# Kernel tuning notes

Measured on AMD Instinct MI355X. Metric: run time of the kernel, lower is better.

## Reference

```python
import jax, jax.numpy as jnp
import numpy as np

N_NODES = 40000
N_EDGES = 100000
N_GRAPHS = 1024
C = 32          # output_channels
F_ATOM = 30     # NUMBER_ATOMIC_GRAPH_FEATURES
F_BOND = 11     # NUMBER_BOND_GRAPH_FEATURES
H_EDGE = 128    # hidden width of edge MLP (== batch_size arg)
T = 3           # num_iterations (message passing steps and set2set steps)


def setup_inputs() -> dict:
    key = jax.random.key(0)
    ks = jax.random.split(key, 16)
    s = lambda i, shape, sc=0.1: jax.random.normal(ks[i], shape, jnp.float32) * sc
    return {
        "x": jax.random.normal(ks[0], (N_NODES, F_ATOM), jnp.float32),
        "edge_attr": jax.random.normal(ks[1], (N_EDGES, F_BOND), jnp.float32),
        "edge_index": jax.random.randint(ks[2], (2, N_EDGES), 0, N_NODES),
        "batch": jnp.sort(jax.random.randint(ks[3], (N_NODES,), 0, N_GRAPHS)),
        "lin0_W": s(4, (C, F_ATOM)), "lin0_b": jnp.zeros((C,), jnp.float32),
        "mlp_W1": s(5, (H_EDGE, F_BOND)), "mlp_b1": jnp.zeros((H_EDGE,), jnp.float32),
        "mlp_W2": s(6, (C * C, H_EDGE), 0.02), "mlp_b2": jnp.zeros((C * C,), jnp.float32),
        "root_W": s(7, (C, C)), "conv_b": jnp.zeros((C,), jnp.float32),
        "gru_Wih": s(8, (3 * C, C)), "gru_Whh": s(9, (3 * C, C)),
        "gru_bih": jnp.zeros((3 * C,), jnp.float32), "gru_bhh": jnp.zeros((3 * C,), jnp.float32),
        "lstm_Wih": s(10, (4 * C, 2 * C)), "lstm_Whh": s(11, (4 * C, C)),
        "lstm_bih": jnp.zeros((4 * C,), jnp.float32), "lstm_bhh": jnp.zeros((4 * C,), jnp.float32),
        "lin1_W": s(12, (C, 2 * C)), "lin1_b": jnp.zeros((C,), jnp.float32),
        "lin2_W": s(13, (1, C)), "lin2_b": jnp.zeros((1,), jnp.float32),
    }


def _mpnn(x, edge_attr, lin0_W, lin0_b, mlp_W1, mlp_b1, mlp_W2, mlp_b2,
          root_W, conv_b, gru_Wih, gru_Whh, gru_bih, gru_bhh,
          lstm_Wih, lstm_Whh, lstm_bih, lstm_bhh, lin1_W, lin1_b, lin2_W, lin2_b,
          edge_index, batch):
    src, dst = edge_index[0], edge_index[1]
    out = jax.nn.relu(x @ lin0_W.T + lin0_b)          # [N, C]
    h = out                                           # GRU hidden state
    # edge-conditioned weights (edge_attr is constant across iterations)
    eh = jax.nn.relu(edge_attr @ mlp_W1.T + mlp_b1)
    W_e = (eh @ mlp_W2.T + mlp_b2).reshape(-1, C, C)  # [E, C, C]
    deg = jax.ops.segment_sum(jnp.ones((src.shape[0],), out.dtype), dst, N_NODES)
    denom = jnp.maximum(deg, 1.0)[:, None]
    for _ in range(T):
        # NNConv: gather + per-edge matmul + scatter-mean, plus root weight & bias
        msg = jnp.einsum('ec,eco->eo', out[src], W_e)               # [E, C]
        aggr = jax.ops.segment_sum(msg, dst, N_NODES) / denom       # mean aggr
        m = jax.nn.relu(aggr + out @ root_W + conv_b)
        # single GRU step (torch gate order r, z, n)
        gx = m @ gru_Wih.T + gru_bih
        gh = h @ gru_Whh.T + gru_bhh
        r = jax.nn.sigmoid(gx[:, :C] + gh[:, :C])
        z = jax.nn.sigmoid(gx[:, C:2 * C] + gh[:, C:2 * C])
        n = jnp.tanh(gx[:, 2 * C:] + r * gh[:, 2 * C:])
        h = (1.0 - z) * n + z * h
        out = h
    # Set2Set pooling (torch LSTM gate order i, f, g, o)
    q_star = jnp.zeros((N_GRAPHS, 2 * C), out.dtype)
    hs = jnp.zeros((N_GRAPHS, C), out.dtype)
    cs = jnp.zeros((N_GRAPHS, C), out.dtype)
    for _ in range(T):
        g = q_star @ lstm_Wih.T + lstm_bih + hs @ lstm_Whh.T + lstm_bhh
        i = jax.nn.sigmoid(g[:, :C])
        f = jax.nn.sigmoid(g[:, C:2 * C])
        gg = jnp.tanh(g[:, 2 * C:3 * C])
        o = jax.nn.sigmoid(g[:, 3 * C:])
        cs = f * cs + i * gg
        hs = o * jnp.tanh(cs)                                       # q, [B, C]
        e = jnp.sum(out * hs[batch], axis=-1)                       # [N]
        emax = jax.ops.segment_max(e, batch, N_GRAPHS)
        ee = jnp.exp(e - emax[batch])
        a = ee / jax.ops.segment_sum(ee, batch, N_GRAPHS)[batch]    # segment softmax
        rr = jax.ops.segment_sum(a[:, None] * out, batch, N_GRAPHS)
        q_star = jnp.concatenate([hs, rr], axis=-1)
    y = jax.nn.relu(q_star @ lin1_W.T + lin1_b)
    return y @ lin2_W.T + lin2_b                                    # [B, num_labels]


def reference(x, edge_index, edge_attr, batch, lin0_W, lin0_b, mlp_W1, mlp_b1,
              mlp_W2, mlp_b2, root_W, conv_b, gru_Wih, gru_Whh, gru_bih, gru_bhh,
              lstm_Wih, lstm_Whh, lstm_bih, lstm_bhh, lin1_W, lin1_b, lin2_W, lin2_b):
    return _mpnn(x, edge_attr, lin0_W, lin0_b, mlp_W1, mlp_b1, mlp_W2, mlp_b2,
                 root_W, conv_b, gru_Wih, gru_Whh, gru_bih, gru_bhh,
                 lstm_Wih, lstm_Whh, lstm_bih, lstm_bhh, lin1_W, lin1_b,
                 lin2_W, lin2_b, edge_index, batch)
```

## Files before the change

### kernel.cpp

```cpp
#include <hip/hip_runtime.h>
#include <hip/hip_bf16.h>
#include <cstdint>

#define NN 40000
#define NE 100000
#define NEP 100096
#define NB 1024
#define MAXN 192

typedef _Float16 halfT;
typedef _Float16 half8 __attribute__((ext_vector_type(8)));
typedef float f32x4 __attribute__((ext_vector_type(4)));

static __device__ __forceinline__ float sigf(float x){ return 1.f/(1.f + __expf(-x)); }
static __device__ __forceinline__ float tanh_f(float x){ float e = __expf(2.f * x); return 1.f - 2.f/(e + 1.f); }

__global__ __launch_bounds__(256) void k_zero(float4* __restrict__ p, int n4){
    int i = blockIdx.x * 256 + threadIdx.x;
    if (i < n4) p[i] = make_float4(0.f, 0.f, 0.f, 0.f);
}

__global__ __launch_bounds__(256) void k_setup(
    const float* __restrict__ x, const float* __restrict__ lin0_W, const float* __restrict__ lin0_b,
    const float* __restrict__ ea, const float* __restrict__ W1, const float* __restrict__ b1,
    const float* __restrict__ W2, const float* __restrict__ b2,
    const int* __restrict__ dstA, const int* __restrict__ batch,
    const float* __restrict__ rootW,
    const float* __restrict__ gWih, const float* __restrict__ gWhh,
    const float* __restrict__ lWih, const float* __restrict__ lWhh, const float* __restrict__ lin1_W,
    float* __restrict__ h, halfT* __restrict__ hH, halfT* __restrict__ ehF, halfT* __restrict__ BfF,
    float* __restrict__ deg, halfT* __restrict__ gateB,
    float* __restrict__ lWihT, float* __restrict__ lWhhT, float* __restrict__ lin1T,
    int* __restrict__ starts)
{
    int b = blockIdx.x, tid = threadIdx.x;
    if (b < 1250){
        __shared__ float sW[32 * 30];
        __shared__ float sB[32];
        for (int idx = tid; idx < 960; idx += 256) sW[idx] = lin0_W[idx];
        if (tid < 32) sB[tid] = lin0_b[tid];
        __syncthreads();
        int t8 = b * 256 + tid;
        int i = t8 >> 3, q4 = t8 & 7;
        const float* xr = x + (size_t)i * 30;
        float xv[30];
        #pragma unroll
        for (int f = 0; f < 30; f++) xv[f] = xr[f];
        float r[4];
        #pragma unroll
        for (int cc = 0; cc < 4; cc++){
            int c = q4 * 4 + cc;
            const float* wr = &sW[c * 30];
            float s = sB[c];
            #pragma unroll
            for (int f = 0; f < 30; f++) s += xv[f] * wr[f];
            r[cc] = fmaxf(s, 0.f);
        }
        *(float4*)(h + (size_t)i * 32 + q4 * 4) = *(float4*)r;
        halfT rh[4];
        #pragma unroll
        for (int cc = 0; cc < 4; cc++) rh[cc] = (halfT)r[cc];
        *(uint2*)(hH + (size_t)i * 32 + q4 * 4) = *(uint2*)rh;
    } else if (b < 7506){
        __shared__ float sW1[128 * 11];
        __shared__ float sb1[128];
        for (int idx = tid; idx < 1408; idx += 256) sW1[idx] = W1[idx];
        if (tid < 128) sb1[tid] = b1[tid];
        __syncthreads();
        int t8 = (b - 1250) * 256 + tid;
        int ch = t8 & 63;
        int s4 = (t8 >> 6) & 3;
        int g16 = t8 >> 8;
        int m = ch & 15, q = ch >> 4;
        int e = g16 * 16 + m;
        int kb = 32 * s4 + q * 8;
        halfT v[8];
        if (e < NE){
            const float* xr = ea + (size_t)e * 11;
            float xv[11];
            #pragma unroll
            for (int f = 0; f < 11; f++) xv[f] = xr[f];
            #pragma unroll
            for (int i8 = 0; i8 < 8; i8++){
                int k = kb + i8;
                const float* wr = &sW1[k * 11];
                float s = sb1[k];
                #pragma unroll
                for (int f = 0; f < 11; f++) s += xv[f] * wr[f];
                v[i8] = (halfT)fmaxf(s, 0.f);
            }
        } else {
            #pragma unroll
            for (int i8 = 0; i8 < 8; i8++) v[i8] = (halfT)0.f;
        }
        *(half8*)(ehF + (size_t)t8 * 8) = *(half8*)v;
    } else if (b < 8022){
        int gid = (b - 7506) * 256 + tid;
        int i8 = gid & 7;
        int ch = (gid >> 3) & 63;
        int nt = (gid >> 9) & 1;
        int ks = gid >> 10;
        int m = ch & 15, q = ch >> 4;
        int o = nt * 16 + m;
        float v;
        if (ks < 128){
            int c = ks >> 2;
            int k = 32 * (ks & 3) + q * 8 + i8;
            v = W2[(size_t)(c * 32 + o) * 128 + k];
        } else {
            int c = q * 8 + i8;
            v = b2[c * 32 + o];
        }
        BfF[gid] = (halfT)v;
    } else if (b < 8413){
        int e = (b - 8022) * 256 + tid;
        if (e < NE) atomicAdd(&deg[dstA[e]], 1.f);
    } else if (b < 8493){
        int t = (b - 8413) * 256 + tid;
        if (t < 8192){ int k = t >> 7, j = t & 127; lWihT[t] = lWih[(size_t)j * 64 + k]; }
        else if (t < 12288){ int t2 = t - 8192; int k = t2 >> 7, j = t2 & 127; lWhhT[t2] = lWhh[(size_t)j * 32 + k]; }
        else if (t < 14336){ int t2 = t - 12288; int k = t2 >> 5, c = t2 & 31; lin1T[t2] = lin1_W[(size_t)c * 64 + k]; }
    } else if (b < 8498){
        int g = (b - 8493) * 256 + tid;
        if (g > NB) return;
        int lo = 0, hi = NN;
        while (lo < hi){
            int mid = (lo + hi) >> 1;
            if (batch[mid] < g) lo = mid + 1; else hi = mid;
        }
        starts[g] = lo;
    } else {
        int t = (b - 8498) * 256 + tid;
        if (t >= 7168) return;
        int tile = t >> 9;
        int l = (t >> 3) & 63;
        int i = t & 7;
        int m = l & 15, q = l >> 4;
        int k = q * 8 + i;
        float v;
        if (tile < 2){
            int c = tile * 16 + m;
            v = rootW[(size_t)k * 32 + c];
        } else if (tile < 8){
            int j = (tile - 2) * 16 + m;
            v = gWih[(size_t)j * 32 + k];
        } else {
            int j = (tile - 8) * 16 + m;
            v = gWhh[(size_t)j * 32 + k];
        }
        gateB[t] = (halfT)v;
    }
}

__global__ __launch_bounds__(512, 4) void k_msg4(
    const halfT* __restrict__ ehF, const halfT* __restrict__ BfF,
    const halfT* __restrict__ hH,
    const int* __restrict__ src, const int* __restrict__ dst,
    float* __restrict__ aggr)
{
    __shared__ halfT sB[2][16384];
    int tid = threadIdx.x;
    int l = tid & 63;
    int wid = blockIdx.x * 8 + (tid >> 6);
    int m = l & 15, q = l >> 4;
    int eb = wid * 32;
    half8 pre[4];
    #pragma unroll
    for (int p = 0; p < 4; p++)
        pre[p] = *(const half8*)(BfF + (size_t)(p * 512 + tid) * 8);
    #pragma unroll
    for (int p = 0; p < 4; p++)
        *(half8*)(&sB[0][(p * 512 + tid) * 8]) = pre[p];
    half8 u0[4], u1[4], ub0, ub1;
    {
        int e0 = eb + m;      int se0 = (e0 < NE) ? src[e0] : 0;
        int e1 = eb + 16 + m; int se1 = (e1 < NE) ? src[e1] : 0;
        const halfT* p0 = hH + (size_t)se0 * 32;
        const halfT* p1 = hH + (size_t)se1 * 32;
        #pragma unroll
        for (int j = 0; j < 4; j++){
            u0[j] = *(const half8*)(p0 + j * 8);
            u1[j] = *(const half8*)(p1 + j * 8);
        }
        ub0 = *(const half8*)(p0 + q * 8);
        ub1 = *(const half8*)(p1 + q * 8);
    }
    half8 eh0[4], eh1[4];
    {
        int g0 = eb >> 4;
        #pragma unroll
        for (int s = 0; s < 4; s++){
            eh0[s] = *(const half8*)(ehF + ((size_t)(g0 * 4 + s) * 64 + l) * 8);
            eh1[s] = *(const half8*)(ehF + ((size_t)((g0 + 1) * 4 + s) * 64 + l) * 8);
        }
    }
    __syncthreads();
    #pragma unroll
    for (int p = 0; p < 4; p++)
        pre[p] = *(const half8*)(BfF + (size_t)16384 + (size_t)(p * 512 + tid) * 8);
    f32x4 acc00 = {0,0,0,0}, acc01 = {0,0,0,0}, acc10 = {0,0,0,0}, acc11 = {0,0,0,0};
    #pragma unroll
    for (int g = 0; g < 8; g++){
        const int cur = g & 1;
        #pragma unroll
        for (int j = 0; j < 16; j++){
            const int ks = g * 16 + j;
            half8 b0 = *(const half8*)(&sB[cur][(j * 2 + 0) * 512 + l * 8]);
            half8 b1 = *(const half8*)(&sB[cur][(j * 2 + 1) * 512 + l * 8]);
            const int c = ks >> 2, s = ks & 3;
            halfT uc0 = u0[c >> 3][c & 7];
            halfT uc1 = u1[c >> 3][c & 7];
            half8 a0 = eh0[s] * uc0;
            half8 a1 = eh1[s] * uc1;
            acc00 = __builtin_amdgcn_mfma_f32_16x16x32_f16(a0, b0, acc00, 0, 0, 0);
            acc01 = __builtin_amdgcn_mfma_f32_16x16x32_f16(a0, b1, acc01, 0, 0, 0);
            acc10 = __builtin_amdgcn_mfma_f32_16x16x32_f16(a1, b0, acc10, 0, 0, 0);
            acc11 = __builtin_amdgcn_mfma_f32_16x16x32_f16(a1, b1, acc11, 0, 0, 0);
        }
        if (g + 1 < 8){
            #pragma unroll
            for (int p = 0; p < 4; p++)
                *(half8*)(&sB[cur ^ 1][(p * 512 + tid) * 8]) = pre[p];
            if (g + 2 < 8){
                #pragma unroll
                for (int p = 0; p < 4; p++)
                    pre[p] = *(const half8*)(BfF + (size_t)(g + 2) * 16384 + (size_t)(p * 512 + tid) * 8);
            }
        }
        __syncthreads();
    }
    {
        half8 b0 = *(const half8*)(BfF + (size_t)256 * 512 + l * 8);
        half8 b1 = *(const half8*)(BfF + (size_t)257 * 512 + l * 8);
        acc00 = __builtin_amdgcn_mfma_f32_16x16x32_f16(ub0, b0, acc00, 0, 0, 0);
        acc01 = __builtin_amdgcn_mfma_f32_16x16x32_f16(ub0, b1, acc01, 0, 0, 0);
        acc10 = __builtin_amdgcn_mfma_f32_16x16x32_f16(ub1, b0, acc10, 0, 0, 0);
        acc11 = __builtin_amdgcn_mfma_f32_16x16x32_f16(ub1, b1, acc11, 0, 0, 0);
    }
    #pragma unroll
    for (int r = 0; r < 4; r++){
        int ea0 = eb + q * 4 + r;
        if (ea0 < NE){
            int d = dst[ea0];
            atomicAdd(&aggr[(size_t)d * 32 + m],      acc00[r]);
            atomicAdd(&aggr[(size_t)d * 32 + 16 + m], acc01[r]);
        }
        int ea1 = eb + 16 + q * 4 + r;
        if (ea1 < NE){
            int d = dst[ea1];
            atomicAdd(&aggr[(size_t)d * 32 + m],      acc10[r]);
            atomicAdd(&aggr[(size_t)d * 32 + 16 + m], acc11[r]);
        }
    }
}

__global__ __launch_bounds__(256) void k_gru(
    float* __restrict__ aggr, const float* __restrict__ deg,
    float* __restrict__ h, halfT* __restrict__ hH,
    const halfT* __restrict__ gateB,
    const float* __restrict__ gbih, const float* __restrict__ gbhh,
    const float* __restrict__ cb)
{
    __shared__ float hbuf[4][16][33];
    __shared__ float mbuf[4][16][33];
    int tid = threadIdx.x;
    int w = tid >> 6, l = tid & 63;
    int m16 = l & 15, q = l >> 4;
    int nb = blockIdx.x * 64 + w * 16;
    float hv[8];
    const float* hp = h + (size_t)(nb + m16) * 32 + q * 8;
    *(float4*)&hv[0] = *(const float4*)(hp);
    *(float4*)&hv[4] = *(const float4*)(hp + 4);
    half8 h_hi, h_lo;
    #pragma unroll
    for (int i = 0; i < 8; i++){
        halfT hi = (halfT)hv[i];
        h_hi[i] = hi;
        h_lo[i] = (halfT)(hv[i] - (float)hi);
        hbuf[w][m16][q * 8 + i] = hv[i];
    }
    f32x4 macc0 = {0,0,0,0}, macc1 = {0,0,0,0};
    {
        half8 B0 = *(const half8*)(gateB + ((size_t)0 * 64 + l) * 8);
        half8 B1 = *(const half8*)(gateB + ((size_t)1 * 64 + l) * 8);
        macc0 = __builtin_amdgcn_mfma_f32_16x16x32_f16(h_hi, B0, macc0, 0, 0, 0);
        macc0 = __builtin_amdgcn_mfma_f32_16x16x32_f16(h_lo, B0, macc0, 0, 0, 0);
        macc1 = __builtin_amdgcn_mfma_f32_16x16x32_f16(h_hi, B1, macc1, 0, 0, 0);
        macc1 = __builtin_amdgcn_mfma_f32_16x16x32_f16(h_lo, B1, macc1, 0, 0, 0);
    }
    {
        float cb0 = cb[m16], cb1 = cb[16 + m16];
        #pragma unroll
        for (int r = 0; r < 4; r++){
            int nr = q * 4 + r;
            int node = nb + nr;
            float invd = 1.f / fmaxf(deg[node], 1.f);
            size_t a0 = (size_t)node * 32 + m16;
            size_t a1 = a0 + 16;
            float av0 = aggr[a0]; aggr[a0] = 0.f;
            float av1 = aggr[a1]; aggr[a1] = 0.f;
            float mv0 = fmaxf(macc0[r] + av0 * invd + cb0, 0.f);
            float mv1 = fmaxf(macc1[r] + av1 * invd + cb1, 0.f);
            mbuf[w][nr][m16]      = mv0;
            mbuf[w][nr][16 + m16] = mv1;
        }
    }
    __syncthreads();
    half8 m_hi, m_lo;
    #pragma unroll
    for (int i = 0; i < 8; i++){
        float mval = mbuf[w][m16][q * 8 + i];
        halfT hi = (halfT)mval;
        m_hi[i] = hi;
        m_lo[i] = (halfT)(mval - (float)hi);
    }
    f32x4 gx[6], gh[6];
    #pragma unroll
    for (int t = 0; t < 6; t++){ gx[t] = (f32x4){0,0,0,0}; gh[t] = (f32x4){0,0,0,0}; }
    #pragma unroll
    for (int t = 0; t < 6; t++){
        half8 Bx = *(const half8*)(gateB + ((size_t)(2 + t) * 64 + l) * 8);
        half8 Bh = *(const half8*)(gateB + ((size_t)(8 + t) * 64 + l) * 8);
        gx[t] = __builtin_amdgcn_mfma_f32_16x16x32_f16(m_hi, Bx, gx[t], 0, 0, 0);
        gx[t] = __builtin_amdgcn_mfma_f32_16x16x32_f16(m_lo, Bx, gx[t], 0, 0, 0);
        gh[t] = __builtin_amdgcn_mfma_f32_16x16x32_f16(h_hi, Bh, gh[t], 0, 0, 0);
        gh[t] = __builtin_amdgcn_mfma_f32_16x16x32_f16(h_lo, Bh, gh[t], 0, 0, 0);
    }
    #pragma unroll
    for (int t = 0; t < 2; t++){
        int c = t * 16 + m16;
        float bxr = gbih[c],      bhr = gbhh[c];
        float bxz = gbih[32 + c], bhz = gbhh[32 + c];
        float bxn = gbih[64 + c], bhn = gbhh[64 + c];
        #pragma unroll
        for (int r = 0; r < 4; r++){
            int nr = q * 4 + r;
            int node = nb + nr;
            float rr = sigf(gx[t][r] + bxr + gh[t][r] + bhr);
            float zz = sigf(gx[2 + t][r] + bxz + gh[2 + t][r] + bhz);
            float nn = tanh_f(gx[4 + t][r] + bxn + rr * (gh[4 + t][r] + bhn));
            float hq = hbuf[w][nr][c];
            float hnew = (1.f - zz) * nn + zz * hq;
            h[(size_t)node * 32 + c]  = hnew;
            hH[(size_t)node * 32 + c] = (halfT)hnew;
        }
    }
}

__global__ __launch_bounds__(64) void k_s2s(
    const float* __restrict__ h, const int* __restrict__ starts,
    const float* __restrict__ lWihT, const float* __restrict__ lWhhT,
    const float* __restrict__ lbih, const float* __restrict__ lbhh,
    const float* __restrict__ lin1T, const float* __restrict__ lin1_b,
    const float* __restrict__ lin2W, const float* __restrict__ lin2b,
    float* __restrict__ e_buf, float* __restrict__ out)
{
    __shared__ float hl[MAXN * 33];
    __shared__ float al[MAXN];
    __shared__ float hsl[32];
    int g = blockIdx.x, l = threadIdx.x;
    int s0 = starts[g], s1 = starts[g + 1];
    int n = s1 - s0;
    int c = l & 31, grp = l >> 5;
    int nl = (n < MAXN) ? n : MAXN;
    for (int idx = l; idx < nl * 32; idx += 64)
        hl[(idx >> 5) * 33 + (idx & 31)] = h[(size_t)s0 * 32 + idx];
    __syncthreads();
    float qs = 0.f, hsv = 0.f, csv = 0.f;
    for (int t = 0; t < 3; t++){
        float a1 = lbih[l] + lbhh[l];
        float a2 = lbih[l + 64] + lbhh[l + 64];
        #pragma unroll 8
        for (int k = 0; k < 64; k++){
            float qk = __shfl(qs, k);
            a1 += qk * lWihT[k * 128 + l];
            a2 += qk * lWihT[k * 128 + 64 + l];
        }
        #pragma unroll 8
        for (int k = 0; k < 32; k++){
            float hk = __shfl(qs, k);
            a1 += hk * lWhhT[k * 128 + l];
            a2 += hk * lWhhT[k * 128 + 64 + l];
        }
        float gate1 = sigf(a1);
        float gate2 = (l < 32) ? tanhf(a2) : sigf(a2);
        float fv = __shfl(gate1, c + 32);
        float ov = __shfl(gate2, c + 32);
        if (l < 32){
            csv = fv * csv + gate1 * gate2;
            hsv = ov * tanhf(csv);
            hsl[l] = hsv;
        }
        __syncthreads();
        float lmax = -3.4e38f;
        for (int i = l; i < n; i += 64){
            const float* hr = (i < MAXN) ? &hl[i * 33] : &h[(size_t)(s0 + i) * 32];
            float p = 0.f;
            #pragma unroll
            for (int c2 = 0; c2 < 32; c2++) p += hr[c2] * hsl[c2];
            if (i < MAXN) al[i] = p; else e_buf[s0 + i] = p;
            lmax = fmaxf(lmax, p);
        }
        #pragma unroll
        for (int o = 1; o < 64; o <<= 1) lmax = fmaxf(lmax, __shfl_xor(lmax, o));
        float lsum = 0.f;
        for (int i = l; i < n; i += 64){
            float e = (i < MAXN) ? al[i] : e_buf[s0 + i];
            float a = expf(e - lmax);
            if (i < MAXN) al[i] = a; else e_buf[s0 + i] = a;
            lsum += a;
        }
        #pragma unroll
        for (int o = 1; o < 64; o <<= 1) lsum += __shfl_xor(lsum, o);
        float inv = (lsum > 0.f) ? 1.f / lsum : 0.f;
        __syncthreads();
        float acc = 0.f;
        for (int i = grp; i < n; i += 2){
            float a = (i < MAXN) ? al[i] : e_buf[s0 + i];
            const float* hr = (i < MAXN) ? &hl[i * 33] : &h[(size_t)(s0 + i) * 32];
            acc += a * hr[c];
        }
        acc *= inv;
        acc += __shfl_xor(acc, 32);
        qs = (l < 32) ? hsv : acc;
        __syncthreads();
    }
    float s = lin1_b[c];
    #pragma unroll 8
    for (int k = 0; k < 64; k++){
        float qk = __shfl(qs, k);
        s += qk * lin1T[k * 32 + c];
    }
    float pp = (l < 32) ? fmaxf(s, 0.f) * lin2W[c] : 0.f;
    pp += __shfl_xor(pp, 1);  pp += __shfl_xor(pp, 2);
    pp += __shfl_xor(pp, 4);  pp += __shfl_xor(pp, 8);
    pp += __shfl_xor(pp, 16); pp += __shfl_xor(pp, 32);
    if (l == 0) out[g] = pp + lin2b[0];
}

extern "C" void kernel_launch(void* const* d_in, const int* in_sizes, int n_in,
                              void* d_out, int out_size, void* d_ws, size_t ws_size,
                              hipStream_t stream){
    (void)in_sizes; (void)n_in; (void)out_size;
    const float* x        = (const float*)d_in[0];
    const float* ea       = (const float*)d_in[1];
    const int*   ei       = (const int*)d_in[2];
    const int*   batch    = (const int*)d_in[3];
    const float* lin0_W   = (const float*)d_in[4];
    const float* lin0_b   = (const float*)d_in[5];
    const float* mlp_W1   = (const float*)d_in[6];
    const float* mlp_b1   = (const float*)d_in[7];
    const float* mlp_W2   = (const float*)d_in[8];
    const float* mlp_b2   = (const float*)d_in[9];
    const float* root_W   = (const float*)d_in[10];
    const float* conv_b   = (const float*)d_in[11];
    const float* gWih     = (const float*)d_in[12];
    const float* gWhh     = (const float*)d_in[13];
    const float* gbih     = (const float*)d_in[14];
    const float* gbhh     = (const float*)d_in[15];
    const float* lWih     = (const float*)d_in[16];
    const float* lWhh     = (const float*)d_in[17];
    const float* lbih     = (const float*)d_in[18];
    const float* lbhh     = (const float*)d_in[19];
    const float* lin1_W   = (const float*)d_in[20];
    const float* lin1_b   = (const float*)d_in[21];
    const float* lin2_W   = (const float*)d_in[22];
    const float* lin2_b   = (const float*)d_in[23];
    const int* src = ei;
    const int* dst = ei + NE;
    float* out = (float*)d_out;

    char* w = (char*)d_ws;
    size_t off = 0;
    auto alloc = [&](size_t bytes) -> void* {
        void* p = w + off;
        off = (off + bytes + 255) & ~(size_t)255;
        return p;
    };
    float* deg    = (float*)alloc((size_t)NN * 4);
    float* aggr   = (float*)alloc((size_t)NN * 32 * 4);
    float* h      = (float*)alloc((size_t)NN * 32 * 4);
    halfT* hH     = (halfT*)alloc((size_t)NN * 32 * 2);
    halfT* ehF    = (halfT*)alloc((size_t)NEP * 128 * 2);
    halfT* BfF    = (halfT*)alloc((size_t)129 * 2 * 64 * 8 * 2);
    int*   starts = (int*)alloc((size_t)(NB + 1) * 4);
    halfT* gateB  = (halfT*)alloc((size_t)14 * 64 * 8 * 2);
    float* lWihT  = (float*)alloc((size_t)8192 * 4);
    float* lWhhT  = (float*)alloc((size_t)4096 * 4);
    float* lin1T  = (float*)alloc((size_t)2048 * 4);
    float* e_buf  = (float*)alloc((size_t)NN * 4);
    if (ws_size < off) return;

    k_zero<<<(330000 + 255) / 256, 256, 0, stream>>>((float4*)deg, 330000);

    k_setup<<<8526, 256, 0, stream>>>(x, lin0_W, lin0_b, ea, mlp_W1, mlp_b1,
        mlp_W2, mlp_b2, dst, batch, root_W, gWih, gWhh, lWih, lWhh, lin1_W,
        h, hH, ehF, BfF, deg, gateB, lWihT, lWhhT, lin1T, starts);

    for (int t = 0; t < 3; t++){
        k_msg4<<<NEP / 256, 512, 0, stream>>>(ehF, BfF, hH, src, dst, aggr);
        k_gru<<<NN / 64, 256, 0, stream>>>(aggr, deg, h, hH, gateB,
                                           gbih, gbhh, conv_b);
    }
    k_s2s<<<NB, 64, 0, stream>>>(h, starts, lWihT, lWhhT, lbih, lbhh,
                                 lin1T, lin1_b, lin2_W, lin2_b, e_buf, out);
}
```

Measured before the change: 183.8 us.

## Retile edge-message MFMA so wave pairs split output columns over 64 edges

Each wave in the message kernel now handles 64 edges (four 16-edge tiles) for one 16-column half of the output, with two waves sharing an edge group, instead of 32 edges by 32 columns. This halves the shared-memory B reads per wave per MFMA and makes each B fragment serve four MFMAs, but it duplicates the per-edge eh/h gathers and the A-operand scaling across the two waves. Register use rises (16 eh and 16 u vectors), so the launch bound occupancy hint drops from 4 to 2 blocks. The block now covers 256 edges, so the grid size presumably has to change to match.

```diff
diff --git a/kernel.cpp b/kernel.cpp
--- a/kernel.cpp
+++ b/kernel.cpp
@@ -152,7 +152,7 @@
     }
 }
 
-__global__ __launch_bounds__(512, 4) void k_msg4(
+__global__ __launch_bounds__(512, 2) void k_msg4(
     const halfT* __restrict__ ehF, const halfT* __restrict__ BfF,
     const halfT* __restrict__ hH,
     const int* __restrict__ src, const int* __restrict__ dst,
@@ -161,9 +161,10 @@
     __shared__ halfT sB[2][16384];
     int tid = threadIdx.x;
     int l = tid & 63;
-    int wid = blockIdx.x * 8 + (tid >> 6);
+    int w = tid >> 6;
+    int eg = w >> 1, nt = w & 1;
     int m = l & 15, q = l >> 4;
-    int eb = wid * 32;
+    int eb = blockIdx.x * 256 + eg * 64;
     half8 pre[4];
     #pragma unroll
     for (int p = 0; p < 4; p++)
@@ -171,51 +172,46 @@
     #pragma unroll
     for (int p = 0; p < 4; p++)
         *(half8*)(&sB[0][(p * 512 + tid) * 8]) = pre[p];
-    half8 u0[4], u1[4], ub0, ub1;
-    {
-        int e0 = eb + m;      int se0 = (e0 < NE) ? src[e0] : 0;
-        int e1 = eb + 16 + m; int se1 = (e1 < NE) ? src[e1] : 0;
-        const halfT* p0 = hH + (size_t)se0 * 32;
-        const halfT* p1 = hH + (size_t)se1 * 32;
-        #pragma unroll
-        for (int j = 0; j < 4; j++){
-            u0[j] = *(const half8*)(p0 + j * 8);
-            u1[j] = *(const half8*)(p1 + j * 8);
-        }
-        ub0 = *(const half8*)(p0 + q * 8);
-        ub1 = *(const half8*)(p1 + q * 8);
-    }
-    half8 eh0[4], eh1[4];
+    int se[4];
+    half8 u[4][4];
+    #pragma unroll
+    for (int T = 0; T < 4; T++){
+        int e = eb + T * 16 + m;
+        se[T] = (e < NE) ? src[e] : 0;
+        const halfT* p0 = hH + (size_t)se[T] * 32;
+        #pragma unroll
+        for (int j = 0; j < 4; j++)
+            u[T][j] = *(const half8*)(p0 + j * 8);
+    }
+    half8 eh[4][4];
     {
         int g0 = eb >> 4;
         #pragma unroll
-        for (int s = 0; s < 4; s++){
-            eh0[s] = *(const half8*)(ehF + ((size_t)(g0 * 4 + s) * 64 + l) * 8);
-            eh1[s] = *(const half8*)(ehF + ((size_t)((g0 + 1) * 4 + s) * 64 + l) * 8);
-        }
+        for (int T = 0; T < 4; T++)
+            #pragma unroll
+            for (int s = 0; s < 4; s++)
+                eh[T][s] = *(const half8*)(ehF + ((size_t)((g0 + T) * 4 + s) * 64 + l) * 8);
     }
     __syncthreads();
     #pragma unroll
     for (int p = 0; p < 4; p++)
         pre[p] = *(const half8*)(BfF + (size_t)16384 + (size_t)(p * 512 + tid) * 8);
-    f32x4 acc00 = {0,0,0,0}, acc01 = {0,0,0,0}, acc10 = {0,0,0,0}, acc11 = {0,0,0,0};
+    f32x4 acc[4];
+    #pragma unroll
+    for (int T = 0; T < 4; T++) acc[T] = (f32x4){0,0,0,0};
     #pragma unroll
     for (int g = 0; g < 8; g++){
         const int cur = g & 1;
         #pragma unroll
         for (int j = 0; j < 16; j++){
             const int ks = g * 16 + j;
-            half8 b0 = *(const half8*)(&sB[cur][(j * 2 + 0) * 512 + l * 8]);
-            half8 b1 = *(const half8*)(&sB[cur][(j * 2 + 1) * 512 + l * 8]);
+            half8 b = *(const half8*)(&sB[cur][((j * 2 + nt) * 512) + l * 8]);
             const int c = ks >> 2, s = ks & 3;
-            halfT uc0 = u0[c >> 3][c & 7];
-            halfT uc1 = u1[c >> 3][c & 7];
-            half8 a0 = eh0[s] * uc0;
-            half8 a1 = eh1[s] * uc1;
-            acc00 = __builtin_amdgcn_mfma_f32_16x16x32_f16(a0, b0, acc00, 0, 0, 0);
-            acc01 = __builtin_amdgcn_mfma_f32_16x16x32_f16(a0, b1, acc01, 0, 0, 0);
-            acc10 = __builtin_amdgcn_mfma_f32_16x16x32_f16(a1, b0, acc10, 0, 0, 0);
-            acc11 = __builtin_amdgcn_mfma_f32_16x16x32_f16(a1, b1, acc11, 0, 0, 0);
+            #pragma unroll
+            for (int T = 0; T < 4; T++){
+                half8 a = eh[T][s] * u[T][c >> 3][c & 7];
+                acc[T] = __builtin_amdgcn_mfma_f32_16x16x32_f16(a, b, acc[T], 0, 0, 0);
+            }
         }
         if (g + 1 < 8){
             #pragma unroll
@@ -230,28 +226,23 @@
         __syncthreads();
     }
     {
-        half8 b0 = *(const half8*)(BfF + (size_t)256 * 512 + l * 8);
-        half8 b1 = *(const half8*)(BfF + (size_t)257 * 512 + l * 8);
-        acc00 = __builtin_amdgcn_mfma_f32_16x16x32_f16(ub0, b0, acc00, 0, 0, 0);
-        acc01 = __builtin_amdgcn_mfma_f32_16x16x32_f16(ub0, b1, acc01, 0, 0, 0);
-        acc10 = __builtin_amdgcn_mfma_f32_16x16x32_f16(ub1, b0, acc10, 0, 0, 0);
-        acc11 = __builtin_amdgcn_mfma_f32_16x16x32_f16(ub1, b1, acc11, 0, 0, 0);
-    }
-    #pragma unroll
-    for (int r = 0; r < 4; r++){
-        int ea0 = eb + q * 4 + r;
-        if (ea0 < NE){
-            int d = dst[ea0];
-            atomicAdd(&aggr[(size_t)d * 32 + m],      acc00[r]);
-            atomicAdd(&aggr[(size_t)d * 32 + 16 + m], acc01[r]);
-        }
-        int ea1 = eb + 16 + q * 4 + r;
-        if (ea1 < NE){
-            int d = dst[ea1];
-            atomicAdd(&aggr[(size_t)d * 32 + m],      acc10[r]);
-            atomicAdd(&aggr[(size_t)d * 32 + 16 + m], acc11[r]);
-        }
-    }
+        half8 b = *(const half8*)(BfF + (size_t)(256 + nt) * 512 + l * 8);
+        #pragma unroll
+        for (int T = 0; T < 4; T++){
+            half8 ub = *(const half8*)(hH + (size_t)se[T] * 32 + q * 8);
+            acc[T] = __builtin_amdgcn_mfma_f32_16x16x32_f16(ub, b, acc[T], 0, 0, 0);
+        }
+    }
+    #pragma unroll
+    for (int T = 0; T < 4; T++)
+        #pragma unroll
+        for (int r = 0; r < 4; r++){
+            int e = eb + T * 16 + q * 4 + r;
+            if (e < NE){
+                int d = dst[e];
+                atomicAdd(&aggr[(size_t)d * 32 + nt * 16 + m], acc[T][r]);
+            }
+        }
 }
 
 __global__ __launch_bounds__(256) void k_gru(
```

Measured after the change: 250.5 us. 1.36x slower.
